# Performance work log

Hardware: AMD Instinct MI355X
Metric: run time of the kernel (lower is better)

## Reference

```python
import jax, jax.numpy as jnp
import numpy as np

N = 50000      # nodes
E = 600000     # edges
D_IN = 128
D = 128        # embedding_size
H = 2 * D      # GENConv MLP hidden (expansion=2, num_layers=2)
L = 6          # gnn_layers
OUT = 2        # out_channels
EPS_MSG = 1e-7   # GENConv message eps
EPS_SM = 1e-16   # PyG softmax denominator eps
LN_EPS = 1e-5


def setup_inputs() -> dict:
    key = jax.random.key(0)
    ks = jax.random.split(key, 18)
    s_in = 1.0 / np.sqrt(D_IN)
    s_d = 1.0 / np.sqrt(D)
    s_h = 1.0 / np.sqrt(H)
    return {
        "x": jax.random.normal(ks[0], (N, D_IN), jnp.float32),
        "edge_index": jax.random.randint(ks[1], (2, E), 0, N, jnp.int64),
        # node encoder
        "enc_W": jax.random.normal(ks[2], (D_IN, D), jnp.float32) * s_in,
        "enc_b": jnp.zeros((D,), jnp.float32),
        # per-layer DeepGCN params (stacked over L layers)
        "ln_g": jnp.ones((L, D), jnp.float32),
        "ln_b": jnp.zeros((L, D), jnp.float32),
        "t": jnp.ones((L,), jnp.float32),  # learnable softmax temperature
        "W1": jax.random.normal(ks[3], (L, D, H), jnp.float32) * s_d,
        "b1": jnp.zeros((L, H), jnp.float32),
        "mln_g": jnp.ones((L, H), jnp.float32),
        "mln_b": jnp.zeros((L, H), jnp.float32),
        "W2": jax.random.normal(ks[4], (L, H, D), jnp.float32) * s_h,
        "b2": jnp.zeros((L, D), jnp.float32),
        # final MLP head (linear_layers=2)
        "lin_W1": jax.random.normal(ks[5], (D, D), jnp.float32) * s_d,
        "lin_b1": jnp.zeros((D,), jnp.float32),
        "lin_W2": jax.random.normal(ks[6], (D, OUT), jnp.float32) * s_d,
        "lin_b2": jnp.zeros((OUT,), jnp.float32),
    }


def _layernorm(h, g, b):
    mu = jnp.mean(h, axis=-1, keepdims=True)
    var = jnp.mean(jnp.square(h - mu), axis=-1, keepdims=True)
    return (h - mu) * jax.lax.rsqrt(var + LN_EPS) * g + b


def _genconv(h, src, dst, t, W1, b1, mg, mb, W2, b2):
    """GENConv with softmax aggregation: gather -> segment softmax -> scatter -> MLP."""
    msg = jax.nn.relu(h[src]) + EPS_MSG            # [E, D]
    scaled = msg * t
    mmax = jax.ops.segment_max(scaled, dst, num_segments=N)  # [N, D]
    mmax = jnp.where(jnp.isfinite(mmax), mmax, 0.0)          # empty segments
    ex = jnp.exp(scaled - mmax[dst])                          # [E, D]
    denom = jax.ops.segment_sum(ex, dst, num_segments=N)     # [N, D]
    alpha = ex / (denom[dst] + EPS_SM)
    agg = jax.ops.segment_sum(msg * alpha, dst, num_segments=N)  # [N, D]
    out = agg + h                                  # root/self term
    z = out @ W1 + b1                              # [N, 2D]
    z = jax.nn.relu(_layernorm(z, mg, mb))
    return z @ W2 + b2                             # [N, D]


def reference(x, edge_index, enc_W, enc_b, ln_g, ln_b, t, W1, b1,
              mln_g, mln_b, W2, b2, lin_W1, lin_b1, lin_W2, lin_b2):
    src, dst = edge_index[0], edge_index[1]
    h = x @ enc_W + enc_b                          # node encoder [N, D]
    for i in range(L):                             # DeepGCNLayer 'res+' blocks
        g = _layernorm(h, ln_g[i], ln_b[i])
        g = jax.nn.relu(g)                         # (dropout: inference no-op)
        g = _genconv(g, src, dst, t[i], W1[i], b1[i], mln_g[i], mln_b[i], W2[i], b2[i])
        h = h + g
    h = jax.nn.relu(h @ lin_W1 + lin_b1)           # head (dropout_rate=None)
    return h @ lin_W2 + lin_b2                     # [N, OUT]
```

## Files before the change

### kernel.cpp

```cpp
#include <hip/hip_runtime.h>

#define NN 50000
#define EE 600000
#define DD 128
#define HH 256
#define LL 6
#define NB 49

typedef _Float16 f16x8 __attribute__((ext_vector_type(8)));
typedef float f32x4 __attribute__((ext_vector_type(4)));

__device__ __forceinline__ float bf2f(unsigned short u){
  unsigned int x = ((unsigned int)u) << 16; float f; __builtin_memcpy(&f, &x, 4); return f;
}
__device__ __forceinline__ unsigned short f2bf(float f){
  unsigned int x; __builtin_memcpy(&x, &f, 4);
  unsigned int lsb = (x >> 16) & 1u; x += 0x7fffu + lsb; return (unsigned short)(x >> 16);
}
__device__ __forceinline__ float wave_sum(float v){
  #pragma unroll
  for (int off = 32; off >= 1; off >>= 1) v += __shfl_xor(v, off, 64);
  return v;
}
__device__ __forceinline__ unsigned short f2h(float f){
  _Float16 h = (_Float16)f; unsigned short u; __builtin_memcpy(&u, &h, 2); return u;
}
__device__ __forceinline__ float h2f(unsigned short u){
  _Float16 h; __builtin_memcpy(&h, &u, 2); return (float)h;
}

__global__ void k_detect(const unsigned short* __restrict__ xh,
                         const unsigned int* __restrict__ ew,
                         int* __restrict__ flags){
  __shared__ int s_bad, s_nz;
  int t = threadIdx.x;
  if (t == 0){ s_bad = 0; s_nz = 0; }
  __syncthreads();
  int bad = 0;
  for (int i = t; i < 512; i += 256){
    unsigned e = (xh[i] >> 7) & 0xffu;
    if (e < 96u || e > 135u) bad = 1;
  }
  if (bad) atomicOr(&s_bad, 1);
  int nz = 0;
  for (int i = t; i < 1024; i += 256)
    if ((i & 1) && ew[i] != 0u) nz = 1;
  if (nz) atomicOr(&s_nz, 1);
  __syncthreads();
  if (t == 0){
    flags[0] = s_bad ? 1 : 0;
    flags[1] = s_nz ? 0 : 1;
  }
}

__global__ void k_cvt_edges(const void* __restrict__ ei, const int* __restrict__ flags,
                            int* __restrict__ s32, int* __restrict__ d32){
  int e = blockIdx.x*256 + threadIdx.x;
  if (e >= EE) return;
  int sv, dv;
  if (flags[1]){
    const long long* p = (const long long*)ei;
    sv = (int)p[e]; dv = (int)p[EE + e];
  } else {
    const int* p = (const int*)ei;
    sv = p[e]; dv = p[EE + e];
  }
  s32[e] = ((unsigned)sv < (unsigned)NN) ? sv : 0;
  d32[e] = ((unsigned)dv < (unsigned)NN) ? dv : 0;
}

__global__ void k_hist(const int* __restrict__ dst, int* __restrict__ deg){
  int e = blockIdx.x*256 + threadIdx.x;
  if (e < EE) atomicAdd(&deg[dst[e]], 1);
}

__global__ void k_blocksum(const int* __restrict__ deg, int* __restrict__ bsum){
  __shared__ int ws[4];
  int t = threadIdx.x, b = blockIdx.x;
  int s = 0;
  int i0 = b*1024 + t*4;
  #pragma unroll
  for (int j=0;j<4;j++){ int i = i0+j; if (i < NN) s += deg[i]; }
  #pragma unroll
  for (int off=32; off>=1; off>>=1) s += __shfl_xor(s, off, 64);
  if ((t&63)==0) ws[t>>6] = s;
  __syncthreads();
  if (t==0) bsum[b] = ws[0]+ws[1]+ws[2]+ws[3];
}

__global__ void k_scanb(const int* __restrict__ bsum, int* __restrict__ boff, int* __restrict__ rowptr){
  int lane = threadIdx.x;
  int v = (lane < NB) ? bsum[lane] : 0;
  int inc = v;
  #pragma unroll
  for (int off=1; off<64; off<<=1){ int u = __shfl_up(inc, off, 64); if (lane>=off) inc += u; }
  if (lane < NB) boff[lane] = inc - v;
  if (lane == 63) rowptr[NN] = inc;
}

__global__ void k_scanscatter(const int* __restrict__ deg, const int* __restrict__ boff,
                              int* __restrict__ rowptr, int* __restrict__ pos){
  __shared__ int ws[4];
  int t = threadIdx.x, b = blockIdx.x;
  int lane = t & 63, wid = t >> 6;
  int i0 = b*1024 + t*4;
  int d[4];
  #pragma unroll
  for (int j=0;j<4;j++){ int i=i0+j; d[j] = (i<NN)? deg[i] : 0; }
  int tot = d[0]+d[1]+d[2]+d[3];
  int inc = tot;
  #pragma unroll
  for (int off=1; off<64; off<<=1){ int u = __shfl_up(inc, off, 64); if (lane>=off) inc += u; }
  if (lane==63) ws[wid] = inc;
  __syncthreads();
  int woff = 0;
  for (int w=0; w<wid; w++) woff += ws[w];
  int base = boff[b] + woff + (inc - tot);
  int pre = 0;
  #pragma unroll
  for (int j=0;j<4;j++){
    int i = i0+j;
    if (i<NN){ rowptr[i] = base + pre; pos[i] = base + pre; }
    pre += d[j];
  }
}

__global__ void k_fill(const int* __restrict__ src, const int* __restrict__ dst,
                       int* __restrict__ pos, int* __restrict__ csr){
  int e = blockIdx.x*256 + threadIdx.x;
  if (e < EE){
    int d = dst[e];
    int p = atomicAdd(&pos[d], 1);
    csr[p] = src[e];
  }
}

__global__ void k_prep_w(const int* __restrict__ flags,
    const void* __restrict__ encW, const void* __restrict__ linW1,
    const void* __restrict__ W1, const void* __restrict__ W2,
    unsigned short* __restrict__ ph, unsigned short* __restrict__ pl)
{
  int idx = blockIdx.x*256 + threadIdx.x;
  int fp32 = flags[0];
  const void* src; int off;
  if (idx < 16384){ int n=idx>>7, k=idx&127; src=encW; off=k*128+n; }
  else if (idx < 32768){ int o=idx-16384; int n=o>>7, k=o&127; src=linW1; off=k*128+n; }
  else if (idx < 229376){ int o=idx-32768; int l=o>>15, r=o&32767; int n=r>>7, k=r&127; src=W1; off=l*32768+k*256+n; }
  else { int o=idx-229376; int l=o>>15, r=o&32767; int n=r>>8, k=r&255; src=W2; off=l*32768+k*128+n; }
  float w = fp32 ? ((const float*)src)[off] : bf2f(((const unsigned short*)src)[off]);
  unsigned short h = f2h(w);
  ph[idx] = h;
  pl[idx] = f2h(w - h2f(h));
}

#define SM_ENCB 0
#define SM_LNG 128
#define SM_LNB 896
#define SM_TV 1664
#define SM_B1 1670
#define SM_MG 3206
#define SM_MB 4742
#define SM_B2 6278
#define SM_LINB1 7046
#define SM_LINW2 7174
#define SM_LINB2 7430
#define SM_TOT 7432
__global__ void k_prep_small(const int* __restrict__ flags,
    const void* s0, const void* s1, const void* s2, const void* s3,
    const void* s4, const void* s5, const void* s6, const void* s7,
    const void* s8, const void* s9, const void* s10, float* __restrict__ out)
{
  int i = blockIdx.x*256 + threadIdx.x;
  if (i >= SM_TOT) return;
  int fp32 = flags[0];
  const void* src; int off;
  if      (i < SM_LNG)  { src=s0;  off=i; }
  else if (i < SM_LNB)  { src=s1;  off=i-SM_LNG; }
  else if (i < SM_TV)   { src=s2;  off=i-SM_LNB; }
  else if (i < SM_B1)   { src=s3;  off=i-SM_TV; }
  else if (i < SM_MG)   { src=s4;  off=i-SM_B1; }
  else if (i < SM_MB)   { src=s5;  off=i-SM_MG; }
  else if (i < SM_B2)   { src=s6;  off=i-SM_MB; }
  else if (i < SM_LINB1){ src=s7;  off=i-SM_B2; }
  else if (i < SM_LINW2){ src=s8;  off=i-SM_LINB1; }
  else if (i < SM_LINB2){ src=s9;  off=i-SM_LINW2; }
  else                  { src=s10; off=i-SM_LINB2; }
  out[i] = fp32 ? ((const float*)src)[off] : bf2f(((const unsigned short*)src)[off]);
}

__device__ __forceinline__ void emit_me(unsigned short* me, int row, int col, float g, float tv){
  float m = g + 1e-7f;
  me[(size_t)row*256 + col] = f2h(m);
  me[(size_t)row*256 + 128 + col] = f2h(__expf(fminf(m*tv, 18.f) - 8.f));
}

template<int EPI>
__global__ __launch_bounds__(256, 4) void k_gemm(const void* __restrict__ Ap,
    const unsigned short* __restrict__ WTh, const unsigned short* __restrict__ WTl,
    const float* __restrict__ bias, void* __restrict__ Cv,
    int M, const int* __restrict__ flags, int aExt)
{
  __shared__ __align__(16) short lA[64*72];
  __shared__ __align__(16) short lW[128*72];

  const int tid = threadIdx.x, lane = tid & 63, wid = tid >> 6;
  const int mi = lane & 15, q = lane >> 4;
  const int rowb = blockIdx.x * 64;
  const int fp32m = flags[0];

  f32x4 acc[4][2];
  #pragma unroll
  for (int a=0;a<4;a++)
    #pragma unroll
    for (int c=0;c<2;c++){ acc[a][c][0]=0.f; acc[a][c][1]=0.f; acc[a][c][2]=0.f; acc[a][c][3]=0.f; }

  const int nW = fp32m ? 2 : 1;
  for (int pass = 0; pass < nW; ++pass){
    const unsigned short* Wp = pass ? WTl : WTh;
    for (int kc = 0; kc < 2; ++kc){
      {
        const int kv = (tid & 7) * 8, r0 = tid >> 3;
        #pragma unroll
        for (int p = 0; p < 2; ++p){
          int row = p*32 + r0, grow = rowb + row;
          uint4 d = make_uint4(0u,0u,0u,0u);
          if (grow < M){
            if (!aExt){
              d = *(const uint4*)((const unsigned short*)Ap + (size_t)grow*128 + kc*64 + kv);
            } else if (!fp32m){
              uint4 u = *(const uint4*)((const unsigned short*)Ap + (size_t)grow*128 + kc*64 + kv);
              const unsigned short* us = (const unsigned short*)&u;
              unsigned short hh[8];
              #pragma unroll
              for (int c=0;c<8;c++) hh[c] = f2h(bf2f(us[c]));
              d.x = hh[0]|((unsigned)hh[1]<<16); d.y = hh[2]|((unsigned)hh[3]<<16);
              d.z = hh[4]|((unsigned)hh[5]<<16); d.w = hh[6]|((unsigned)hh[7]<<16);
            } else {
              const float* fp = (const float*)Ap + (size_t)grow*128 + kc*64 + kv;
              float4 v0 = *(const float4*)fp, v1 = *(const float4*)(fp+4);
              unsigned short hh[8] = {f2h(v0.x),f2h(v0.y),f2h(v0.z),f2h(v0.w),
                                      f2h(v1.x),f2h(v1.y),f2h(v1.z),f2h(v1.w)};
              d.x = hh[0]|((unsigned)hh[1]<<16); d.y = hh[2]|((unsigned)hh[3]<<16);
              d.z = hh[4]|((unsigned)hh[5]<<16); d.w = hh[6]|((unsigned)hh[7]<<16);
            }
          }
          *(uint4*)&lA[row*72 + kv] = d;
        }
        #pragma unroll
        for (int p = 0; p < 4; ++p){
          int n = p*32 + r0;
          *(uint4*)&lW[n*72 + kv] = *(const uint4*)(Wp + (size_t)n*128 + kc*64 + kv);
        }
      }
      __syncthreads();
      #pragma unroll
      for (int ks = 0; ks < 2; ++ks){
        const int koff = ks*32 + q*8;
        f16x8 af[4], bw[2];
        #pragma unroll
        for (int rt=0; rt<4; rt++) af[rt] = *(const f16x8*)&lA[(rt*16+mi)*72 + koff];
        #pragma unroll
        for (int ct=0; ct<2; ct++) bw[ct] = *(const f16x8*)&lW[(wid*32 + ct*16 + mi)*72 + koff];
        #pragma unroll
        for (int rt=0; rt<4; rt++)
          #pragma unroll
          for (int ct=0; ct<2; ct++)
            acc[rt][ct] = __builtin_amdgcn_mfma_f32_16x16x32_f16(af[rt], bw[ct], acc[rt][ct], 0,0,0);
      }
      __syncthreads();
    }
  }
  #pragma unroll
  for (int ct=0; ct<2; ct++){
    const int col = wid*32 + ct*16 + mi;
    const float bf = bias[col];
    #pragma unroll
    for (int rt=0; rt<4; rt++)
      #pragma unroll
      for (int r=0; r<4; r++){
        int row = rowb + rt*16 + q*4 + r;
        if (row < M){
          float v = acc[rt][ct][r] + bf;
          if (EPI == 1) v = fmaxf(v, 0.f);
          if (EPI == 3) ((unsigned short*)Cv)[(size_t)row*128 + col] = f2h(v);
          else          ((float*)Cv)[(size_t)row*128 + col] = v;
        }
      }
  }
}

__global__ __launch_bounds__(256, 3) void k_gemm1(const unsigned short* __restrict__ Ap,
    const unsigned short* __restrict__ WTh, const unsigned short* __restrict__ WTl,
    const float* __restrict__ bias, const float* __restrict__ gam, const float* __restrict__ bet,
    unsigned short* __restrict__ z, int M, const int* __restrict__ flags)
{
  __shared__ __align__(16) short lA[64*72];
  __shared__ __align__(16) short lW[256*72];
  __shared__ float2 sred[4][64];

  const int tid = threadIdx.x, lane = tid & 63, wid = tid >> 6;
  const int mi = lane & 15, q = lane >> 4;
  const int rowb = blockIdx.x * 64;

  f32x4 acc[4][4];
  #pragma unroll
  for (int a=0;a<4;a++)
    #pragma unroll
    for (int c=0;c<4;c++){ acc[a][c][0]=0.f; acc[a][c][1]=0.f; acc[a][c][2]=0.f; acc[a][c][3]=0.f; }

  const int nW = flags[0] ? 2 : 1;
  for (int pass = 0; pass < nW; ++pass){
    const unsigned short* Wp = pass ? WTl : WTh;
    for (int kc = 0; kc < 2; ++kc){
      {
        const int kv = (tid & 7) * 8, r0 = tid >> 3;
        #pragma unroll
        for (int p = 0; p < 2; ++p){
          int row = p*32 + r0, grow = rowb + row;
          uint4 d = make_uint4(0u,0u,0u,0u);
          if (grow < M) d = *(const uint4*)(Ap + (size_t)grow*128 + kc*64 + kv);
          *(uint4*)&lA[row*72 + kv] = d;
        }
        #pragma unroll
        for (int p = 0; p < 8; ++p){
          int n = p*32 + r0;
          *(uint4*)&lW[n*72 + kv] = *(const uint4*)(Wp + (size_t)n*128 + kc*64 + kv);
        }
      }
      __syncthreads();
      #pragma unroll
      for (int ks = 0; ks < 2; ++ks){
        const int koff = ks*32 + q*8;
        f16x8 af[4], bw[4];
        #pragma unroll
        for (int rt=0; rt<4; rt++) af[rt] = *(const f16x8*)&lA[(rt*16+mi)*72 + koff];
        #pragma unroll
        for (int ct=0; ct<4; ct++) bw[ct] = *(const f16x8*)&lW[(wid*64 + ct*16 + mi)*72 + koff];
        #pragma unroll
        for (int rt=0; rt<4; rt++)
          #pragma unroll
          for (int ct=0; ct<4; ct++)
            acc[rt][ct] = __builtin_amdgcn_mfma_f32_16x16x32_f16(af[rt], bw[ct], acc[rt][ct], 0,0,0);
      }
      __syncthreads();
    }
  }
  #pragma unroll
  for (int ct=0; ct<4; ct++){
    const float bf = bias[wid*64 + ct*16 + mi];
    #pragma unroll
    for (int rt=0; rt<4; rt++)
      #pragma unroll
      for (int r=0; r<4; r++) acc[rt][ct][r] += bf;
  }
  #pragma unroll
  for (int rt=0; rt<4; rt++)
    #pragma unroll
    for (int r=0; r<4; r++){
      float s = 0.f, s2 = 0.f;
      #pragma unroll
      for (int ct=0; ct<4; ct++){ float v = acc[rt][ct][r]; s += v; s2 += v*v; }
      #pragma unroll
      for (int off=1; off<16; off<<=1){ s += __shfl_xor(s, off, 64); s2 += __shfl_xor(s2, off, 64); }
      if (mi == 0) sred[wid][rt*16 + q*4 + r] = make_float2(s, s2);
    }
  __syncthreads();
  #pragma unroll
  for (int rt=0; rt<4; rt++)
    #pragma unroll
    for (int r=0; r<4; r++){
      int rl = rt*16 + q*4 + r;
      float2 t0 = sred[0][rl], t1 = sred[1][rl], t2 = sred[2][rl], t3 = sred[3][rl];
      float s = t0.x + t1.x + t2.x + t3.x;
      float s2 = t0.y + t1.y + t2.y + t3.y;
      float m = s * (1.f/256.f);
      float var = s2 * (1.f/256.f) - m*m;
      float rs = rsqrtf(var + 1e-5f);
      int row = rowb + rl;
      if (row < M){
        #pragma unroll
        for (int ct=0; ct<4; ct++){
          int col = wid*64 + ct*16 + mi;
          float v = (acc[rt][ct][r] - m) * rs * gam[col] + bet[col];
          z[(size_t)row*256 + col] = f2h(fmaxf(v, 0.f));
        }
      }
    }
}

__global__ __launch_bounds__(256, 4) void k_gemm2(const unsigned short* __restrict__ Ap,
    const unsigned short* __restrict__ WTh, const unsigned short* __restrict__ WTl,
    const float* __restrict__ bias, unsigned short* __restrict__ h16,
    const float* __restrict__ gam, const float* __restrict__ bet,
    const float* __restrict__ tp,
    unsigned short* __restrict__ me,
    int M, const int* __restrict__ flags, int doLN)
{
  __shared__ __align__(16) short lA[64*72];
  __shared__ __align__(16) short lW[128*72];
  __shared__ float2 sred[4][64];

  const int tid = threadIdx.x, lane = tid & 63, wid = tid >> 6;
  const int mi = lane & 15, q = lane >> 4;
  const int rowb = blockIdx.x * 64;
  const float tv = tp[0];

  f32x4 acc[4][2];
  #pragma unroll
  for (int a=0;a<4;a++)
    #pragma unroll
    for (int c=0;c<2;c++){ acc[a][c][0]=0.f; acc[a][c][1]=0.f; acc[a][c][2]=0.f; acc[a][c][3]=0.f; }

  const int nW = flags[0] ? 2 : 1;
  for (int pass = 0; pass < nW; ++pass){
    const unsigned short* Wp = pass ? WTl : WTh;
    for (int kc = 0; kc < 4; ++kc){
      {
        const int kv = (tid & 7) * 8, r0 = tid >> 3;
        #pragma unroll
        for (int p = 0; p < 2; ++p){
          int row = p*32 + r0, grow = rowb + row;
          uint4 d = make_uint4(0u,0u,0u,0u);
          if (grow < M) d = *(const uint4*)(Ap + (size_t)grow*256 + kc*64 + kv);
          *(uint4*)&lA[row*72 + kv] = d;
        }
        #pragma unroll
        for (int p = 0; p < 4; ++p){
          int n = p*32 + r0;
          *(uint4*)&lW[n*72 + kv] = *(const uint4*)(Wp + (size_t)n*256 + kc*64 + kv);
        }
      }
      __syncthreads();
      #pragma unroll
      for (int ks = 0; ks < 2; ++ks){
        const int koff = ks*32 + q*8;
        f16x8 af[4], bw[2];
        #pragma unroll
        for (int rt=0; rt<4; rt++) af[rt] = *(const f16x8*)&lA[(rt*16+mi)*72 + koff];
        #pragma unroll
        for (int ct=0; ct<2; ct++) bw[ct] = *(const f16x8*)&lW[(wid*32 + ct*16 + mi)*72 + koff];
        #pragma unroll
        for (int rt=0; rt<4; rt++)
          #pragma unroll
          for (int ct=0; ct<2; ct++)
            acc[rt][ct] = __builtin_amdgcn_mfma_f32_16x16x32_f16(af[rt], bw[ct], acc[rt][ct], 0,0,0);
      }
      __syncthreads();
    }
  }
  #pragma unroll
  for (int ct=0; ct<2; ct++){
    const int col = wid*32 + ct*16 + mi;
    const float bf = bias[col];
    #pragma unroll
    for (int rt=0; rt<4; rt++)
      #pragma unroll
      for (int r=0; r<4; r++){
        int row = rowb + rt*16 + q*4 + r;
        if (row < M){
          float hv = acc[rt][ct][r] + bf + h2f(h16[(size_t)row*128 + col]);
          h16[(size_t)row*128 + col] = f2h(hv);
          acc[rt][ct][r] = hv;
        }
      }
  }
  if (!doLN) return;
  #pragma unroll
  for (int rt=0; rt<4; rt++)
    #pragma unroll
    for (int r=0; r<4; r++){
      float s = 0.f, s2 = 0.f;
      #pragma unroll
      for (int ct=0; ct<2; ct++){ float v = acc[rt][ct][r]; s += v; s2 += v*v; }
      #pragma unroll
      for (int off=1; off<16; off<<=1){ s += __shfl_xor(s, off, 64); s2 += __shfl_xor(s2, off, 64); }
      if (mi == 0) sred[wid][rt*16 + q*4 + r] = make_float2(s, s2);
    }
  __syncthreads();
  #pragma unroll
  for (int rt=0; rt<4; rt++)
    #pragma unroll
    for (int r=0; r<4; r++){
      int rl = rt*16 + q*4 + r;
      float2 t0 = sred[0][rl], t1 = sred[1][rl], t2 = sred[2][rl], t3 = sred[3][rl];
      float s = t0.x + t1.x + t2.x + t3.x;
      float s2 = t0.y + t1.y + t2.y + t3.y;
      float m = s * (1.f/128.f);
      float var = s2 * (1.f/128.f) - m*m;
      float rs = rsqrtf(var + 1e-5f);
      int row = rowb + rl;
      if (row < M){
        #pragma unroll
        for (int ct=0; ct<2; ct++){
          int col = wid*32 + ct*16 + mi;
          float g = fmaxf((acc[rt][ct][r] - m) * rs * gam[col] + bet[col], 0.f);
          emit_me(me, row, col, g, tv);
        }
      }
    }
}

__global__ __launch_bounds__(256,4) void k_preln0(const unsigned short* __restrict__ h16,
    const float* __restrict__ gam, const float* __restrict__ bet,
    const float* __restrict__ tp, unsigned short* __restrict__ me)
{
  int wid = threadIdx.x >> 6, lane = threadIdx.x & 63;
  int row = blockIdx.x*4 + wid;
  float tv = tp[0];
  unsigned u = ((const unsigned*)(h16 + (size_t)row*DD))[lane];
  float v0 = h2f((unsigned short)(u & 0xffffu));
  float v1 = h2f((unsigned short)(u >> 16));
  float mean = wave_sum(v0+v1) * (1.f/128.f);
  float d0 = v0-mean, d1 = v1-mean;
  float var = wave_sum(d0*d0 + d1*d1) * (1.f/128.f);
  float rs = rsqrtf(var + 1e-5f);
  float o0 = fmaxf(d0*rs*gam[2*lane]   + bet[2*lane],   0.f);
  float o1 = fmaxf(d1*rs*gam[2*lane+1] + bet[2*lane+1], 0.f);
  emit_me(me, row, 2*lane,   o0, tv);
  emit_me(me, row, 2*lane+1, o1, tv);
}

__global__ __launch_bounds__(256,4) void k_agg(
    const unsigned short* __restrict__ me,
    const int* __restrict__ rowptr, const int* __restrict__ csr,
    unsigned short* __restrict__ obf)
{
  int wid = threadIdx.x>>6, lane = threadIdx.x&63;
  int node = blockIdx.x*4 + wid;
  int st = rowptr[node], en = rowptr[node+1];
  int quad = lane >> 4, fi = lane & 15;
  float l[8], ac[8];
  #pragma unroll
  for (int f=0; f<8; f++){ l[f]=0.f; ac[f]=0.f; }
  for (int base = st; base < en; base += 64){
    int cnt = min(64, en - base);
    int sv = (lane < cnt) ? csr[base + lane] : NN;
    for (int j = 0; j < cnt; j += 8){
      int s0i = __shfl(sv, j + quad, 64);
      int s1i = __shfl(sv, j + 4 + quad, 64);
      bool two = (j + 4) < cnt;
      const unsigned short* mer0 = me + (size_t)s0i*256 + fi*8;
      f16x8 mh0 = *(const f16x8*)(mer0);
      f16x8 eh0 = *(const f16x8*)(mer0 + 128);
      if (two){
        const unsigned short* mer1 = me + (size_t)s1i*256 + fi*8;
        f16x8 mh1 = *(const f16x8*)(mer1);
        f16x8 eh1 = *(const f16x8*)(mer1 + 128);
        #pragma unroll
        for (int f=0; f<8; f++){
          l[f]  = fmaf((float)eh0[f], 1.f, l[f]);
          ac[f] = fmaf((float)mh0[f], (float)eh0[f], ac[f]);
          l[f]  = fmaf((float)eh1[f], 1.f, l[f]);
          ac[f] = fmaf((float)mh1[f], (float)eh1[f], ac[f]);
        }
      } else {
        #pragma unroll
        for (int f=0; f<8; f++){
          l[f]  = fmaf((float)eh0[f], 1.f, l[f]);
          ac[f] = fmaf((float)mh0[f], (float)eh0[f], ac[f]);
        }
      }
    }
  }
  #pragma unroll
  for (int off=16; off<=32; off<<=1)
    #pragma unroll
    for (int f=0; f<8; f++){ l[f] += __shfl_xor(l[f], off, 64); ac[f] += __shfl_xor(ac[f], off, 64); }
  if (quad == 0){
    f16x8 mh = *(const f16x8*)(me + (size_t)node*256 + fi*8);
    unsigned short o[8];
    #pragma unroll
    for (int f=0; f<8; f++){
      float a = ac[f] / (l[f] + 1e-16f);
      o[f] = f2h(((float)mh[f] - 1e-7f) + a);
    }
    uint4 w;
    w.x = o[0]|((unsigned)o[1]<<16); w.y = o[2]|((unsigned)o[3]<<16);
    w.z = o[4]|((unsigned)o[5]<<16); w.w = o[6]|((unsigned)o[7]<<16);
    *(uint4*)(obf + (size_t)node*DD + fi*8) = w;
  }
}

__global__ __launch_bounds__(256,4) void k_head2(const float* __restrict__ u,
    const float* __restrict__ w, const float* __restrict__ b,
    void* __restrict__ out, const int* __restrict__ flags)
{
  int wid = threadIdx.x>>6, lane = threadIdx.x&63;
  int row = blockIdx.x*4 + wid;
  const float* ur = u + (size_t)row*DD;
  float u0 = ur[lane], u1 = ur[lane+64];
  float s0 = u0*w[lane*2+0] + u1*w[(lane+64)*2+0];
  float s1 = u0*w[lane*2+1] + u1*w[(lane+64)*2+1];
  s0 = wave_sum(s0); s1 = wave_sum(s1);
  if (lane == 0){
    float o0 = s0 + b[0], o1 = s1 + b[1];
    if (flags[0]){
      ((float*)out)[row*2+0] = o0;
      ((float*)out)[row*2+1] = o1;
    } else {
      ((unsigned short*)out)[row*2+0] = f2bf(o0);
      ((unsigned short*)out)[row*2+1] = f2bf(o1);
    }
  }
}

extern "C" void kernel_launch(void* const* d_in, const int* in_sizes, int n_in,
                              void* d_out, int out_size, void* d_ws, size_t ws_size,
                              hipStream_t stream)
{
  (void)in_sizes; (void)n_in; (void)out_size; (void)ws_size;
  char* ws = (char*)d_ws;
  size_t off = 0;
  auto alloc = [&](size_t bytes) -> char* {
    char* p = ws + off;
    off = (off + bytes + 255) & ~(size_t)255;
    return p;
  };
  int* flags  = (int*)alloc(256);
  float* sm   = (float*)alloc(SM_TOT*4);
  unsigned short* planeH = (unsigned short*)alloc(425984*2);
  unsigned short* planeL = (unsigned short*)alloc(425984*2);
  int* src32  = (int*)alloc((size_t)EE*4);
  int* dst32  = (int*)alloc((size_t)EE*4);
  int* deg    = (int*)alloc((size_t)NN*4);
  int* pos    = (int*)alloc((size_t)NN*4);
  int* rowptr = (int*)alloc((size_t)(NN+1)*4);
  int* csr    = (int*)alloc((size_t)EE*4);
  int* bsum   = (int*)alloc(64*4);
  int* boff   = (int*)alloc(64*4);
  unsigned short* h16 = (unsigned short*)alloc((size_t)NN*128*2);
  unsigned short* z    = (unsigned short*)alloc((size_t)NN*256*2);
  unsigned short* me   = (unsigned short*)alloc((size_t)(NN+1)*256*2);
  unsigned short* obf  = (unsigned short*)alloc((size_t)NN*128*2);
  float* ob   = (float*)alloc((size_t)NN*128*4);

  k_detect<<<1,256,0,stream>>>((const unsigned short*)d_in[0], (const unsigned int*)d_in[1], flags);
  k_cvt_edges<<<(EE+255)/256,256,0,stream>>>(d_in[1], flags, src32, dst32);
  hipMemsetAsync(deg, 0, (size_t)NN*4, stream);
  hipMemsetAsync(me + (size_t)NN*256, 0, 512, stream);
  k_hist<<<(EE+255)/256,256,0,stream>>>(dst32, deg);
  k_blocksum<<<NB,256,0,stream>>>(deg, bsum);
  k_scanb<<<1,64,0,stream>>>(bsum, boff, rowptr);
  k_scanscatter<<<NB,256,0,stream>>>(deg, boff, rowptr, pos);
  k_fill<<<(EE+255)/256,256,0,stream>>>(src32, dst32, pos, csr);
  k_prep_w<<<1664,256,0,stream>>>(flags, d_in[2], d_in[13], d_in[7], d_in[11], planeH, planeL);
  k_prep_small<<<30,256,0,stream>>>(flags, d_in[3], d_in[4], d_in[5], d_in[6], d_in[8],
                                    d_in[9], d_in[10], d_in[12], d_in[14], d_in[15], d_in[16], sm);

  const int GB = (NN + 63)/64;
  k_gemm<3><<<GB,256,0,stream>>>((const void*)d_in[0], planeH + 0, planeL + 0,
                                 sm + SM_ENCB, (void*)h16, NN, flags, 1);
  k_preln0<<<NN/4,256,0,stream>>>(h16, sm + SM_LNG, sm + SM_LNB, sm + SM_TV, me);
  for (int i = 0; i < LL; ++i){
    k_agg<<<NN/4,256,0,stream>>>(me, rowptr, csr, obf);
    k_gemm1<<<GB,256,0,stream>>>(obf, planeH + 32768 + i*32768, planeL + 32768 + i*32768,
                                 sm + SM_B1 + i*256, sm + SM_MG + i*256, sm + SM_MB + i*256,
                                 z, NN, flags);
    int nl = (i+1 < LL) ? (i+1) : 0;
    k_gemm2<<<GB,256,0,stream>>>(z, planeH + 229376 + i*32768, planeL + 229376 + i*32768,
                                 sm + SM_B2 + i*128, h16,
                                 sm + SM_LNG + nl*128, sm + SM_LNB + nl*128,
                                 sm + SM_TV + nl,
                                 me, NN, flags, (i+1 < LL) ? 1 : 0);
  }
  k_gemm<1><<<GB,256,0,stream>>>((const void*)h16, planeH + 16384, planeL + 16384,
                                 sm + SM_LINB1, (void*)ob, NN, flags, 0);
  k_head2<<<NN/4,256,0,stream>>>(ob, sm + SM_LINW2, sm + SM_LINB2, d_out, flags);
}
```

Baseline: 884.1 us.

## Fuse GENConv MLP GEMMs into one kernel keeping hidden activations in LDS

Merges the two per-layer MLP GEMM kernels into a single k_layer kernel. The 256-wide hidden activation after LayerNorm+ReLU is written to shared memory instead of a global z buffer, and the second GEMM reads it from there. This removes a global round trip of an N×256 fp16 tensor and one launch per layer. Shared memory per block grows to about 51KB, which can lower occupancy, and the second GEMM now runs under the first kernel's 3-block launch bound.

New measurement: 883.8 us. No clear change (-0.0%).

```diff
diff --git a/kernel.cpp b/kernel.cpp
--- a/kernel.cpp
+++ b/kernel.cpp
@@ -289,31 +289,39 @@
   }
 }
 
-__global__ __launch_bounds__(256, 3) void k_gemm1(const unsigned short* __restrict__ Ap,
-    const unsigned short* __restrict__ WTh, const unsigned short* __restrict__ WTl,
-    const float* __restrict__ bias, const float* __restrict__ gam, const float* __restrict__ bet,
-    unsigned short* __restrict__ z, int M, const int* __restrict__ flags)
-{
-  __shared__ __align__(16) short lA[64*72];
-  __shared__ __align__(16) short lW[256*72];
-  __shared__ float2 sred[4][64];
+__global__ __launch_bounds__(256, 3) void k_layer(const unsigned short* __restrict__ Ap,
+    const unsigned short* __restrict__ W1h, const unsigned short* __restrict__ W1l,
+    const unsigned short* __restrict__ W2h, const unsigned short* __restrict__ W2l,
+    const float* __restrict__ b1, const float* __restrict__ mg, const float* __restrict__ mb,
+    const float* __restrict__ b2, unsigned short* __restrict__ h16,
+    const float* __restrict__ gam, const float* __restrict__ bet,
+    const float* __restrict__ tp, unsigned short* __restrict__ me,
+    int M, const int* __restrict__ flags, int doLN)
+{
+  __shared__ __align__(16) char smem[52224];
+  short* lA  = (short*)smem;
+  short* lW1 = (short*)(smem + 9216);
+  short* zT  = (short*)smem;
+  short* lW2 = (short*)(smem + 33792);
+  float2* sred = (float2*)smem;
 
   const int tid = threadIdx.x, lane = tid & 63, wid = tid >> 6;
   const int mi = lane & 15, q = lane >> 4;
+  const int kv = (tid & 7) * 8, r0 = tid >> 3;
   const int rowb = blockIdx.x * 64;
-
-  f32x4 acc[4][4];
+  const float tv = tp[0];
+  const int nW = flags[0] ? 2 : 1;
+
+  f32x4 acc1[4][4];
   #pragma unroll
   for (int a=0;a<4;a++)
     #pragma unroll
-    for (int c=0;c<4;c++){ acc[a][c][0]=0.f; acc[a][c][1]=0.f; acc[a][c][2]=0.f; acc[a][c][3]=0.f; }
-
-  const int nW = flags[0] ? 2 : 1;
+    for (int c=0;c<4;c++){ acc1[a][c][0]=0.f; acc1[a][c][1]=0.f; acc1[a][c][2]=0.f; acc1[a][c][3]=0.f; }
+
   for (int pass = 0; pass < nW; ++pass){
-    const unsigned short* Wp = pass ? WTl : WTh;
+    const unsigned short* Wp = pass ? W1l : W1h;
     for (int kc = 0; kc < 2; ++kc){
-      {
-        const int kv = (tid & 7) * 8, r0 = tid >> 3;
+      if (pass == 0){
         #pragma unroll
         for (int p = 0; p < 2; ++p){
           int row = p*32 + r0, grow = rowb + row;
@@ -321,11 +329,11 @@
           if (grow < M) d = *(const uint4*)(Ap + (size_t)grow*128 + kc*64 + kv);
           *(uint4*)&lA[row*72 + kv] = d;
         }
-        #pragma unroll
-        for (int p = 0; p < 8; ++p){
-          int n = p*32 + r0;
-          *(uint4*)&lW[n*72 + kv] = *(const uint4*)(Wp + (size_t)n*128 + kc*64 + kv);
-        }
+      }
+      #pragma unroll
+      for (int p = 0; p < 8; ++p){
+        int n = p*32 + r0;
+        *(uint4*)&lW1[n*72 + kv] = *(const uint4*)(Wp + (size_t)n*128 + kc*64 + kv);
       }
       __syncthreads();
       #pragma unroll
@@ -335,23 +343,23 @@
         #pragma unroll
         for (int rt=0; rt<4; rt++) af[rt] = *(const f16x8*)&lA[(rt*16+mi)*72 + koff];
         #pragma unroll
-        for (int ct=0; ct<4; ct++) bw[ct] = *(const f16x8*)&lW[(wid*64 + ct*16 + mi)*72 + koff];
+        for (int ct=0; ct<4; ct++) bw[ct] = *(const f16x8*)&lW1[(wid*64 + ct*16 + mi)*72 + koff];
         #pragma unroll
         for (int rt=0; rt<4; rt++)
           #pragma unroll
           for (int ct=0; ct<4; ct++)
-            acc[rt][ct] = __builtin_amdgcn_mfma_f32_16x16x32_f16(af[rt], bw[ct], acc[rt][ct], 0,0,0);
+            acc1[rt][ct] = __builtin_amdgcn_mfma_f32_16x16x32_f16(af[rt], bw[ct], acc1[rt][ct], 0,0,0);
       }
       __syncthreads();
     }
   }
   #pragma unroll
   for (int ct=0; ct<4; ct++){
-    const float bf = bias[wid*64 + ct*16 + mi];
+    const float bf = b1[wid*64 + ct*16 + mi];
     #pragma unroll
     for (int rt=0; rt<4; rt++)
       #pragma unroll
-      for (int r=0; r<4; r++) acc[rt][ct][r] += bf;
+      for (int r=0; r<4; r++) acc1[rt][ct][r] += bf;
   }
   #pragma unroll
   for (int rt=0; rt<4; rt++)
@@ -359,76 +367,54 @@
     for (int r=0; r<4; r++){
       float s = 0.f, s2 = 0.f;
       #pragma unroll
-      for (int ct=0; ct<4; ct++){ float v = acc[rt][ct][r]; s += v; s2 += v*v; }
+      for (int ct=0; ct<4; ct++){ float v = acc1[rt][ct][r]; s += v; s2 += v*v; }
       #pragma unroll
       for (int off=1; off<16; off<<=1){ s += __shfl_xor(s, off, 64); s2 += __shfl_xor(s2, off, 64); }
-      if (mi == 0) sred[wid][rt*16 + q*4 + r] = make_float2(s, s2);
-    }
-  __syncthreads();
+      if (mi == 0) sred[wid*64 + rt*16 + q*4 + r] = make_float2(s, s2);
+    }
+  __syncthreads();
+  float lnm[4][4], lnr[4][4];
   #pragma unroll
   for (int rt=0; rt<4; rt++)
     #pragma unroll
     for (int r=0; r<4; r++){
       int rl = rt*16 + q*4 + r;
-      float2 t0 = sred[0][rl], t1 = sred[1][rl], t2 = sred[2][rl], t3 = sred[3][rl];
+      float2 t0 = sred[0*64+rl], t1 = sred[1*64+rl], t2 = sred[2*64+rl], t3 = sred[3*64+rl];
       float s = t0.x + t1.x + t2.x + t3.x;
       float s2 = t0.y + t1.y + t2.y + t3.y;
       float m = s * (1.f/256.f);
       float var = s2 * (1.f/256.f) - m*m;
-      float rs = rsqrtf(var + 1e-5f);
-      int row = rowb + rl;
-      if (row < M){
-        #pragma unroll
-        for (int ct=0; ct<4; ct++){
-          int col = wid*64 + ct*16 + mi;
-          float v = (acc[rt][ct][r] - m) * rs * gam[col] + bet[col];
-          z[(size_t)row*256 + col] = f2h(fmaxf(v, 0.f));
-        }
-      }
-    }
-}
-
-__global__ __launch_bounds__(256, 4) void k_gemm2(const unsigned short* __restrict__ Ap,
-    const unsigned short* __restrict__ WTh, const unsigned short* __restrict__ WTl,
-    const float* __restrict__ bias, unsigned short* __restrict__ h16,
-    const float* __restrict__ gam, const float* __restrict__ bet,
-    const float* __restrict__ tp,
-    unsigned short* __restrict__ me,
-    int M, const int* __restrict__ flags, int doLN)
-{
-  __shared__ __align__(16) short lA[64*72];
-  __shared__ __align__(16) short lW[128*72];
-  __shared__ float2 sred[4][64];
-
-  const int tid = threadIdx.x, lane = tid & 63, wid = tid >> 6;
-  const int mi = lane & 15, q = lane >> 4;
-  const int rowb = blockIdx.x * 64;
-  const float tv = tp[0];
-
-  f32x4 acc[4][2];
+      lnm[rt][r] = m;
+      lnr[rt][r] = rsqrtf(var + 1e-5f);
+    }
+  __syncthreads();
+  #pragma unroll
+  for (int ct=0; ct<4; ct++){
+    const int col = wid*64 + ct*16 + mi;
+    const float gc = mg[col], bc = mb[col];
+    #pragma unroll
+    for (int rt=0; rt<4; rt++)
+      #pragma unroll
+      for (int r=0; r<4; r++){
+        int rl = rt*16 + q*4 + r;
+        float v = (acc1[rt][ct][r] - lnm[rt][r]) * lnr[rt][r] * gc + bc;
+        zT[rl*264 + col] = (short)f2h(fmaxf(v, 0.f));
+      }
+  }
+  __syncthreads();
+  f32x4 acc2[4][2];
   #pragma unroll
   for (int a=0;a<4;a++)
     #pragma unroll
-    for (int c=0;c<2;c++){ acc[a][c][0]=0.f; acc[a][c][1]=0.f; acc[a][c][2]=0.f; acc[a][c][3]=0.f; }
-
-  const int nW = flags[0] ? 2 : 1;
+    for (int c=0;c<2;c++){ acc2[a][c][0]=0.f; acc2[a][c][1]=0.f; acc2[a][c][2]=0.f; acc2[a][c][3]=0.f; }
+
   for (int pass = 0; pass < nW; ++pass){
-    const unsigned short* Wp = pass ? WTl : WTh;
+    const unsigned short* Wp = pass ? W2l : W2h;
     for (int kc = 0; kc < 4; ++kc){
-      {
-        const int kv = (tid & 7) * 8, r0 = tid >> 3;
-        #pragma unroll
-        for (int p = 0; p < 2; ++p){
-          int row = p*32 + r0, grow = rowb + row;
-          uint4 d = make_uint4(0u,0u,0u,0u);
-          if (grow < M) d = *(const uint4*)(Ap + (size_t)grow*256 + kc*64 + kv);
-          *(uint4*)&lA[row*72 + kv] = d;
-        }
-        #pragma unroll
-        for (int p = 0; p < 4; ++p){
-          int n = p*32 + r0;
-          *(uint4*)&lW[n*72 + kv] = *(const uint4*)(Wp + (size_t)n*256 + kc*64 + kv);
-        }
+      #pragma unroll
+      for (int p = 0; p < 4; ++p){
+        int n = p*32 + r0;
+        *(uint4*)&lW2[n*72 + kv] = *(const uint4*)(Wp + (size_t)n*256 + kc*64 + kv);
       }
       __syncthreads();
       #pragma unroll
@@ -436,14 +422,14 @@
         const int koff = ks*32 + q*8;
         f16x8 af[4], bw[2];
         #pragma unroll
-        for (int rt=0; rt<4; rt++) af[rt] = *(const f16x8*)&lA[(rt*16+mi)*72 + koff];
-        #pragma unroll
-        for (int ct=0; ct<2; ct++) bw[ct] = *(const f16x8*)&lW[(wid*32 + ct*16 + mi)*72 + koff];
+        for (int rt=0; rt<4; rt++) af[rt] = *(const f16x8*)&zT[(rt*16+mi)*264 + kc*64 + koff];
+        #pragma unroll
+        for (int ct=0; ct<2; ct++) bw[ct] = *(const f16x8*)&lW2[(wid*32 + ct*16 + mi)*72 + koff];
         #pragma unroll
         for (int rt=0; rt<4; rt++)
           #pragma unroll
           for (int ct=0; ct<2; ct++)
-            acc[rt][ct] = __builtin_amdgcn_mfma_f32_16x16x32_f16(af[rt], bw[ct], acc[rt][ct], 0,0,0);
+            acc2[rt][ct] = __builtin_amdgcn_mfma_f32_16x16x32_f16(af[rt], bw[ct], acc2[rt][ct], 0,0,0);
       }
       __syncthreads();
     }
@@ -451,16 +437,16 @@
   #pragma unroll
   for (int ct=0; ct<2; ct++){
     const int col = wid*32 + ct*16 + mi;
-    const float bf = bias[col];
+    const float bf = b2[col];
     #pragma unroll
     for (int rt=0; rt<4; rt++)
       #pragma unroll
       for (int r=0; r<4; r++){
         int row = rowb + rt*16 + q*4 + r;
         if (row < M){
-          float hv = acc[rt][ct][r] + bf + h2f(h16[(size_t)row*128 + col]);
+          float hv = acc2[rt][ct][r] + bf + h2f(h16[(size_t)row*128 + col]);
           h16[(size_t)row*128 + col] = f2h(hv);
-          acc[rt][ct][r] = hv;
+          acc2[rt][ct][r] = hv;
         }
       }
   }
@@ -471,10 +457,10 @@
     for (int r=0; r<4; r++){
       float s = 0.f, s2 = 0.f;
       #pragma unroll
-      for (int ct=0; ct<2; ct++){ float v = acc[rt][ct][r]; s += v; s2 += v*v; }
+      for (int ct=0; ct<2; ct++){ float v = acc2[rt][ct][r]; s += v; s2 += v*v; }
       #pragma unroll
       for (int off=1; off<16; off<<=1){ s += __shfl_xor(s, off, 64); s2 += __shfl_xor(s2, off, 64); }
-      if (mi == 0) sred[wid][rt*16 + q*4 + r] = make_float2(s, s2);
+      if (mi == 0) sred[wid*64 + rt*16 + q*4 + r] = make_float2(s, s2);
     }
   __syncthreads();
   #pragma unroll
@@ -482,7 +468,7 @@
     #pragma unroll
     for (int r=0; r<4; r++){
       int rl = rt*16 + q*4 + r;
-      float2 t0 = sred[0][rl], t1 = sred[1][rl], t2 = sred[2][rl], t3 = sred[3][rl];
+      float2 t0 = sred[0*64+rl], t1 = sred[1*64+rl], t2 = sred[2*64+rl], t3 = sred[3*64+rl];
       float s = t0.x + t1.x + t2.x + t3.x;
       float s2 = t0.y + t1.y + t2.y + t3.y;
       float m = s * (1.f/128.f);
@@ -493,7 +479,7 @@
         #pragma unroll
         for (int ct=0; ct<2; ct++){
           int col = wid*32 + ct*16 + mi;
-          float g = fmaxf((acc[rt][ct][r] - m) * rs * gam[col] + bet[col], 0.f);
+          float g = fmaxf((acc2[rt][ct][r] - m) * rs * gam[col] + bet[col], 0.f);
           emit_me(me, row, col, g, tv);
         }
       }
@@ -629,7 +615,6 @@
   int* bsum   = (int*)alloc(64*4);
   int* boff   = (int*)alloc(64*4);
   unsigned short* h16 = (unsigned short*)alloc((size_t)NN*128*2);
-  unsigned short* z    = (unsigned short*)alloc((size_t)NN*256*2);
   unsigned short* me   = (unsigned short*)alloc((size_t)(NN+1)*256*2);
   unsigned short* obf  = (unsigned short*)alloc((size_t)NN*128*2);
   float* ob   = (float*)alloc((size_t)NN*128*4);
@@ -653,11 +638,11 @@
   k_preln0<<<NN/4,256,0,stream>>>(h16, sm + SM_LNG, sm + SM_LNB, sm + SM_TV, me);
   for (int i = 0; i < LL; ++i){
     k_agg<<<NN/4,256,0,stream>>>(me, rowptr, csr, obf);
-    k_gemm1<<<GB,256,0,stream>>>(obf, planeH + 32768 + i*32768, planeL + 32768 + i*32768,
+    int nl = (i+1 < LL) ? (i+1) : 0;
+    k_layer<<<GB,256,0,stream>>>(obf,
+                                 planeH + 32768 + i*32768, planeL + 32768 + i*32768,
+                                 planeH + 229376 + i*32768, planeL + 229376 + i*32768,
                                  sm + SM_B1 + i*256, sm + SM_MG + i*256, sm + SM_MB + i*256,
-                                 z, NN, flags);
-    int nl = (i+1 < LL) ? (i+1) : 0;
-    k_gemm2<<<GB,256,0,stream>>>(z, planeH + 229376 + i*32768, planeL + 229376 + i*32768,
                                  sm + SM_B2 + i*128, h16,
                                  sm + SM_LNG + nl*128, sm + SM_LNB + nl*128,
                                  sm + SM_TV + nl,
```
